# Optimization experiments

Hardware: AMD Instinct MI355X
Metric: run time of the kernel (lower is better)

Reference implementation:

```python
import jax, jax.numpy as jnp
import numpy as np

B, L, D = 2, 2048, 1024
H, DH = 16, 64
HIDDEN = 4096
DILATION, WINDOW, CAUSAL = 2, 512, True
EPS = 1e-5


def _ln(x, g, b):
    m = jnp.mean(x, axis=-1, keepdims=True)
    v = jnp.mean(jnp.square(x - m), axis=-1, keepdims=True)
    return (x - m) * jax.lax.rsqrt(v + EPS) * g + b


def setup_inputs() -> dict:
    key = jax.random.key(0)
    ks = jax.random.split(key, 8)
    s = 0.02
    return {
        "x": jax.random.normal(ks[0], (B, L, D), jnp.float32),
        "ln1_g": jnp.ones((D,), jnp.float32),
        "ln1_b": jnp.zeros((D,), jnp.float32),
        "w_qkv": jax.random.normal(ks[1], (3 * D, D), jnp.float32) * s,
        "b_qkv": jnp.zeros((3 * D,), jnp.float32),
        "w_o": jax.random.normal(ks[2], (D, D), jnp.float32) * s,
        "b_o": jnp.zeros((D,), jnp.float32),
        "ln2_g": jnp.ones((D,), jnp.float32),
        "ln2_b": jnp.zeros((D,), jnp.float32),
        "w_ff1": jax.random.normal(ks[3], (HIDDEN, D), jnp.float32) * s,
        "b_ff1": jnp.zeros((HIDDEN,), jnp.float32),
        "w_ff2": jax.random.normal(ks[4], (D, HIDDEN), jnp.float32) * s,
        "b_ff2": jnp.zeros((D,), jnp.float32),
    }


def reference(x, ln1_g, ln1_b, w_qkv, b_qkv, w_o, b_o, ln2_g, ln2_b, w_ff1, b_ff1, w_ff2, b_ff2):
    # pre-norm attention block with dilated/windowed/causal mask
    h = _ln(x, ln1_g, ln1_b)
    qkv = h @ w_qkv.T + b_qkv                      # [B, L, 3D]
    q, k, v = jnp.split(qkv, 3, axis=-1)
    q = q.reshape(B, L, H, DH)
    k = k.reshape(B, L, H, DH)
    v = v.reshape(B, L, H, DH)

    scale = 1.0 / jnp.sqrt(jnp.float32(DH))
    scores = jnp.einsum("bqhd,bkhd->bhqk", q, k) * scale  # [B, H, L, L]

    i = jnp.arange(L)[:, None]
    j = jnp.arange(L)[None, :]
    allowed = ((i - j) % DILATION == 0) & (jnp.abs(i - j) <= WINDOW)
    if CAUSAL:
        allowed = allowed & (j <= i)
    scores = jnp.where(allowed, scores, -jnp.inf)  # diagonal always allowed -> rows finite

    p = jax.nn.softmax(scores, axis=-1)
    attn = jnp.einsum("bhqk,bkhd->bqhd", p, v).reshape(B, L, D)

    out = x + attn @ w_o.T + b_o                   # residual 1 (dropout p=0)

    h2 = _ln(out, ln2_g, ln2_b)
    ff = jax.nn.gelu(h2 @ w_ff1.T + b_ff1, approximate=False) @ w_ff2.T + b_ff2
    return out + ff                                # residual 2
```

## Files before the change

kernel.cpp:

```cpp
#include <hip/hip_runtime.h>
#include <hip/hip_bf16.h>
#include <cmath>

#define Bsz 2
#define Lseq 2048
#define Dmod 1024
#define Hhead 16
#define DH 64
#define HID 4096
#define ROWS (Bsz * Lseq)
#define TD (3 * Dmod)

typedef __attribute__((ext_vector_type(8))) short bf16x8;
typedef __attribute__((ext_vector_type(4))) float f32x4;
typedef unsigned short ushort_t;

typedef const __attribute__((address_space(1))) void gv_t;
typedef __attribute__((address_space(3))) void lv_t;
#define GLDS16(GP, LP) __builtin_amdgcn_global_load_lds((gv_t*)(GP), (lv_t*)(LP), 16, 0, 0)

__device__ __forceinline__ float bf2f(short u)
{
    return __uint_as_float(((unsigned)(unsigned short)u) << 16);
}
__device__ __forceinline__ unsigned pack2(float a, float b)
{
    __hip_bfloat162 t;
    t.x = __float2bfloat16(a);
    t.y = __float2bfloat16(b);
    return *reinterpret_cast<unsigned*>(&t);
}
__device__ __forceinline__ float gelu_exact(float t)
{
    return 0.5f * t * (1.0f + erff(t * 0.70710678118654752f));
}

__device__ __forceinline__ void xcd_remap(int& mblk, int& nblk)
{
    int nx = gridDim.x;
    int nwg = nx * gridDim.y;
    int id = blockIdx.y * nx + blockIdx.x;
    int cpx = nwg >> 3;
    int swz = (id & 7) * cpx + (id >> 3);
    mblk = swz / nx;
    nblk = swz % nx;
}

__global__ __launch_bounds__(256) void f2b_kernel(const float* __restrict__ in,
                                                  ushort_t* __restrict__ out, int n4)
{
    int i = blockIdx.x * 256 + threadIdx.x;
    if (i >= n4) return;
    float4 v = reinterpret_cast<const float4*>(in)[i];
    uint2 o;
    o.x = pack2(v.x, v.y);
    o.y = pack2(v.z, v.w);
    reinterpret_cast<uint2*>(out)[i] = o;
}

__global__ __launch_bounds__(256) void ln_kernel(const float* __restrict__ x,
                                                 const float* __restrict__ g,
                                                 const float* __restrict__ bta,
                                                 ushort_t* __restrict__ out)
{
    int row = blockIdx.x;
    int t = threadIdx.x;
    const float4* xr = reinterpret_cast<const float4*>(x) + (size_t)row * 256;
    float4 v = xr[t];
    float s  = v.x + v.y + v.z + v.w;
    float s2 = v.x * v.x + v.y * v.y + v.z * v.z + v.w * v.w;
#pragma unroll
    for (int o = 32; o > 0; o >>= 1) {
        s  += __shfl_down(s, o);
        s2 += __shfl_down(s2, o);
    }
    __shared__ float sa[4], sb[4];
    int wv = t >> 6, ln = t & 63;
    if (ln == 0) { sa[wv] = s; sb[wv] = s2; }
    __syncthreads();
    s  = sa[0] + sa[1] + sa[2] + sa[3];
    s2 = sb[0] + sb[1] + sb[2] + sb[3];
    float mean = s * (1.0f / 1024.0f);
    float var  = s2 * (1.0f / 1024.0f) - mean * mean;
    float inv  = rsqrtf(var + 1e-5f);
    float4 gv = reinterpret_cast<const float4*>(g)[t];
    float4 bv = reinterpret_cast<const float4*>(bta)[t];
    uint2 o;
    o.x = pack2((v.x - mean) * inv * gv.x + bv.x, (v.y - mean) * inv * gv.y + bv.y);
    o.y = pack2((v.z - mean) * inv * gv.z + bv.z, (v.w - mean) * inv * gv.w + bv.w);
    reinterpret_cast<uint2*>(out)[(size_t)row * 256 + t] = o;
}

__global__ __launch_bounds__(256) void gemm_bt(const ushort_t* __restrict__ A,
                                               const ushort_t* __restrict__ W,
                                               const float* __restrict__ bias,
                                               const float* __restrict__ res,
                                               void* __restrict__ C,
                                               int M, int N, int K, int ldw,
                                               int act, int obf)
{
    __shared__ ushort_t As[128 * 64];
    __shared__ ushort_t Bs[128 * 64];

    int tid = threadIdx.x;
    int w = tid >> 6, lane = tid & 63;
    int mblk, nblk;
    xcd_remap(mblk, nblk);
    int m0 = mblk * 128, n0 = nblk * 128;
    int wr = (w >> 1) * 64, wc = (w & 1) * 64;

    int srow = lane >> 3;
    int scol = (((lane & 7) ^ (lane >> 3)) & 7) * 8;
    const ushort_t* ga[4];
    const ushort_t* gb[4];
    ushort_t* la[4];
    ushort_t* lb[4];
#pragma unroll
    for (int q = 0; q < 4; ++q) {
        ga[q] = A + (size_t)(m0 + w * 32 + q * 8 + srow) * K + scol;
        gb[q] = W + (size_t)(n0 + w * 32 + q * 8 + srow) * ldw + scol;
        la[q] = As + (w * 32 + q * 8) * 64;
        lb[q] = Bs + (w * 32 + q * 8) * 64;
    }

    int fr = lane & 15;
    int fg = lane >> 4;
    int r0 = fg * 4;
    int cc = fr;

    f32x4 acc[4][4] = {};

    for (int k0 = 0; k0 < K; k0 += 64) {
#pragma unroll
        for (int q = 0; q < 4; ++q) {
            GLDS16(ga[q] + k0, la[q]);
            GLDS16(gb[q] + k0, lb[q]);
        }
        __syncthreads();

#pragma unroll
        for (int kk = 0; kk < 2; ++kk) {
            bf16x8 af[4], bfr[4];
#pragma unroll
            for (int i = 0; i < 4; ++i) {
                int ca = ((kk * 4 + fg) ^ (fr & 7)) * 8;
                af[i]  = *reinterpret_cast<const bf16x8*>(&As[(wr + i * 16 + fr) * 64 + ca]);
                bfr[i] = *reinterpret_cast<const bf16x8*>(&Bs[(wc + i * 16 + fr) * 64 + ca]);
            }
#pragma unroll
            for (int mi = 0; mi < 4; ++mi)
#pragma unroll
                for (int ni = 0; ni < 4; ++ni)
                    acc[mi][ni] = __builtin_amdgcn_mfma_f32_16x16x32_bf16(
                        af[mi], bfr[ni], acc[mi][ni], 0, 0, 0);
        }
        __syncthreads();
    }

    float bv[4];
#pragma unroll
    for (int ni = 0; ni < 4; ++ni)
        bv[ni] = bias ? bias[n0 + wc + ni * 16 + cc] : 0.0f;

#pragma unroll
    for (int mi = 0; mi < 4; ++mi) {
#pragma unroll
        for (int r = 0; r < 4; ++r) {
            int row = m0 + wr + mi * 16 + r0 + r;
            const float* resrow = res ? res + (size_t)row * N : nullptr;
#pragma unroll
            for (int ni = 0; ni < 4; ++ni) {
                int col = n0 + wc + ni * 16 + cc;
                float v = acc[mi][ni][r] + bv[ni];
                if (act == 1) v = gelu_exact(v);
                if (resrow) v += resrow[col];
                if (obf) {
                    reinterpret_cast<ushort_t*>(C)[(size_t)row * N + col] =
                        (ushort_t)__bfloat16_as_ushort(__float2bfloat16(v));
                } else {
                    reinterpret_cast<float*>(C)[(size_t)row * N + col] = v;
                }
            }
        }
    }
}

__global__ __launch_bounds__(256) void gemm_n64(const ushort_t* __restrict__ A,
                                                const ushort_t* __restrict__ W,
                                                const float* __restrict__ bias,
                                                const float* __restrict__ res,
                                                void* __restrict__ C,
                                                int M, int N, int K, int ldw,
                                                int act, int obf)
{
    __shared__ ushort_t As[128 * 64];
    __shared__ ushort_t Bs[64 * 64];

    int tid = threadIdx.x;
    int w = tid >> 6, lane = tid & 63;
    int mblk, nblk;
    xcd_remap(mblk, nblk);
    int m0 = mblk * 128, n0 = nblk * 64;
    int wr = (w >> 1) * 64, wc = (w & 1) * 32;

    int srow = lane >> 3;
    int scol = (((lane & 7) ^ (lane >> 3)) & 7) * 8;
    const ushort_t* ga[4];
    const ushort_t* gb[2];
    ushort_t* la[4];
    ushort_t* lb[2];
#pragma unroll
    for (int q = 0; q < 4; ++q) {
        ga[q] = A + (size_t)(m0 + w * 32 + q * 8 + srow) * K + scol;
        la[q] = As + (w * 32 + q * 8) * 64;
    }
#pragma unroll
    for (int q = 0; q < 2; ++q) {
        gb[q] = W + (size_t)(n0 + w * 16 + q * 8 + srow) * ldw + scol;
        lb[q] = Bs + (w * 16 + q * 8) * 64;
    }

    int fr = lane & 15;
    int fg = lane >> 4;
    int r0 = fg * 4;
    int cc = fr;

    f32x4 acc[4][2] = {};

    for (int k0 = 0; k0 < K; k0 += 64) {
#pragma unroll
        for (int q = 0; q < 4; ++q) GLDS16(ga[q] + k0, la[q]);
#pragma unroll
        for (int q = 0; q < 2; ++q) GLDS16(gb[q] + k0, lb[q]);
        __syncthreads();

#pragma unroll
        for (int kk = 0; kk < 2; ++kk) {
            bf16x8 af[4], bfr[2];
            int ca = ((kk * 4 + fg) ^ (fr & 7)) * 8;
#pragma unroll
            for (int i = 0; i < 4; ++i)
                af[i] = *reinterpret_cast<const bf16x8*>(&As[(wr + i * 16 + fr) * 64 + ca]);
#pragma unroll
            for (int i = 0; i < 2; ++i)
                bfr[i] = *reinterpret_cast<const bf16x8*>(&Bs[(wc + i * 16 + fr) * 64 + ca]);
#pragma unroll
            for (int mi = 0; mi < 4; ++mi)
#pragma unroll
                for (int ni = 0; ni < 2; ++ni)
                    acc[mi][ni] = __builtin_amdgcn_mfma_f32_16x16x32_bf16(
                        af[mi], bfr[ni], acc[mi][ni], 0, 0, 0);
        }
        __syncthreads();
    }

    float bv[2];
#pragma unroll
    for (int ni = 0; ni < 2; ++ni)
        bv[ni] = bias ? bias[n0 + wc + ni * 16 + cc] : 0.0f;

#pragma unroll
    for (int mi = 0; mi < 4; ++mi) {
#pragma unroll
        for (int r = 0; r < 4; ++r) {
            int row = m0 + wr + mi * 16 + r0 + r;
            const float* resrow = res ? res + (size_t)row * N : nullptr;
#pragma unroll
            for (int ni = 0; ni < 2; ++ni) {
                int col = n0 + wc + ni * 16 + cc;
                float v = acc[mi][ni][r] + bv[ni];
                if (act == 1) v = gelu_exact(v);
                if (resrow) v += resrow[col];
                if (obf) {
                    reinterpret_cast<ushort_t*>(C)[(size_t)row * N + col] =
                        (ushort_t)__bfloat16_as_ushort(__float2bfloat16(v));
                } else {
                    reinterpret_cast<float*>(C)[(size_t)row * N + col] = v;
                }
            }
        }
    }
}

__global__ __launch_bounds__(256) void attn_mfma(const ushort_t* __restrict__ qkv,
                                                 ushort_t* __restrict__ out)
{
    __shared__ ushort_t Vt[64][328];
    __shared__ ushort_t Pw[4][16][40];

    int bid = blockIdx.x;
    int qt = bid & 15, h = (bid >> 4) & 15, p = (bid >> 8) & 1, b = bid >> 9;
    int qt0 = qt * 64;
    int kstart = qt0 - 256;

    const ushort_t* base = qkv + (size_t)b * Lseq * TD;
    int tid = threadIdx.x;

#pragma unroll
    for (int it = 0; it < 10; ++it) {
        int idx = it * 256 + tid;
        int ko = idx >> 3;
        int dg = idx & 7;
        int kk = kstart + ko;
        bf16x8 v = {};
        if (kk >= 0)
            v = *reinterpret_cast<const bf16x8*>(base + (size_t)(2 * kk + p) * TD + 2048 + h * 64 + dg * 8);
#pragma unroll
        for (int j = 0; j < 8; ++j)
            Vt[dg * 8 + j][ko] = (ushort_t)v[j];
    }

    int w = tid >> 6, lane = tid & 63;
    int fr = lane & 15, fg = lane >> 4;
    int qw = qt0 + w * 16;
    const ushort_t* qrow = base + (size_t)(2 * (qw + fr) + p) * TD + h * 64;
    bf16x8 qf0 = *reinterpret_cast<const bf16x8*>(qrow + fg * 8);
    bf16x8 qf1 = *reinterpret_cast<const bf16x8*>(qrow + 32 + fg * 8);

    __syncthreads();

    float m[4]    = {-1e30f, -1e30f, -1e30f, -1e30f};
    float lsum[4] = {};
    f32x4 o[4]    = {};
    const float scale = 0.125f;
    int qbase = qw + fg * 4;

    for (int t = 0; t < 10; ++t) {
        int kt0 = kstart + t * 32;
        int kk0 = kt0 + fr, kk1 = kk0 + 16;
        int kk0c = kk0 < 0 ? 0 : kk0;
        int kk1c = kk1 < 0 ? 0 : kk1;
        const ushort_t* kr0 = base + (size_t)(2 * kk0c + p) * TD + 1024 + h * 64;
        const ushort_t* kr1 = base + (size_t)(2 * kk1c + p) * TD + 1024 + h * 64;
        bf16x8 k00 = *reinterpret_cast<const bf16x8*>(kr0 + fg * 8);
        bf16x8 k01 = *reinterpret_cast<const bf16x8*>(kr0 + 32 + fg * 8);
        bf16x8 k10 = *reinterpret_cast<const bf16x8*>(kr1 + fg * 8);
        bf16x8 k11 = *reinterpret_cast<const bf16x8*>(kr1 + 32 + fg * 8);

        f32x4 s0 = {}, s1 = {};
        s0 = __builtin_amdgcn_mfma_f32_16x16x32_bf16(qf0, k00, s0, 0, 0, 0);
        s0 = __builtin_amdgcn_mfma_f32_16x16x32_bf16(qf1, k01, s0, 0, 0, 0);
        s1 = __builtin_amdgcn_mfma_f32_16x16x32_bf16(qf0, k10, s1, 0, 0, 0);
        s1 = __builtin_amdgcn_mfma_f32_16x16x32_bf16(qf1, k11, s1, 0, 0, 0);

        int c0 = kt0 + fr, c1 = c0 + 16;
        float v0[4], v1[4], tmax[4];
#pragma unroll
        for (int r = 0; r < 4; ++r) {
            int qq = qbase + r;
            bool a0 = (c0 >= 0) && (c0 <= qq) && (c0 >= qq - 256);
            bool a1 = (c1 >= 0) && (c1 <= qq) && (c1 >= qq - 256);
            v0[r] = a0 ? s0[r] * scale : -1e30f;
            v1[r] = a1 ? s1[r] * scale : -1e30f;
            tmax[r] = fmaxf(v0[r], v1[r]);
        }
#pragma unroll
        for (int off = 1; off < 16; off <<= 1) {
#pragma unroll
            for (int r = 0; r < 4; ++r)
                tmax[r] = fmaxf(tmax[r], __shfl_xor(tmax[r], off));
        }
#pragma unroll
        for (int r = 0; r < 4; ++r) {
            float mn = fmaxf(m[r], tmax[r]);
            float corr = __expf(m[r] - mn);
            m[r] = mn;
            float p0 = __expf(v0[r] - mn);
            float p1 = __expf(v1[r] - mn);
            lsum[r] = lsum[r] * corr + p0 + p1;
#pragma unroll
            for (int db = 0; db < 4; ++db)
                o[db][r] *= corr;
            Pw[w][fg * 4 + r][fr]      = (ushort_t)__bfloat16_as_ushort(__float2bfloat16(p0));
            Pw[w][fg * 4 + r][fr + 16] = (ushort_t)__bfloat16_as_ushort(__float2bfloat16(p1));
        }

        bf16x8 pf = *reinterpret_cast<const bf16x8*>(&Pw[w][fr][fg * 8]);
#pragma unroll
        for (int db = 0; db < 4; ++db) {
            bf16x8 vf = *reinterpret_cast<const bf16x8*>(&Vt[db * 16 + fr][t * 32 + fg * 8]);
            o[db] = __builtin_amdgcn_mfma_f32_16x16x32_bf16(pf, vf, o[db], 0, 0, 0);
        }
    }

#pragma unroll
    for (int off = 1; off < 16; off <<= 1) {
#pragma unroll
        for (int r = 0; r < 4; ++r)
            lsum[r] += __shfl_xor(lsum[r], off);
    }
    float inv[4];
#pragma unroll
    for (int r = 0; r < 4; ++r) inv[r] = 1.0f / lsum[r];

#pragma unroll
    for (int r = 0; r < 4; ++r) {
        size_t orow = ((size_t)b * Lseq + 2 * (qbase + r) + p) * Dmod + h * 64;
#pragma unroll
        for (int db = 0; db < 4; ++db)
            out[orow + db * 16 + fr] =
                (ushort_t)__bfloat16_as_ushort(__float2bfloat16(o[db][r] * inv[r]));
    }
}

extern "C" void kernel_launch(void* const* d_in, const int* in_sizes, int n_in,
                              void* d_out, int out_size, void* d_ws, size_t ws_size,
                              hipStream_t stream)
{
    const float* x     = (const float*)d_in[0];
    const float* ln1_g = (const float*)d_in[1];
    const float* ln1_b = (const float*)d_in[2];
    const float* w_qkv = (const float*)d_in[3];
    const float* b_qkv = (const float*)d_in[4];
    const float* w_o   = (const float*)d_in[5];
    const float* b_o   = (const float*)d_in[6];
    const float* ln2_g = (const float*)d_in[7];
    const float* ln2_b = (const float*)d_in[8];
    const float* w_ff1 = (const float*)d_in[9];
    const float* b_ff1 = (const float*)d_in[10];
    const float* w_ff2 = (const float*)d_in[11];
    const float* b_ff2 = (const float*)d_in[12];
    float* out = (float*)d_out;

    ushort_t* wq     = (ushort_t*)d_ws;
    ushort_t* wo     = wq  + (size_t)TD * Dmod;
    ushort_t* wf1    = wo  + (size_t)Dmod * Dmod;
    ushort_t* wf2    = wf1 + (size_t)HID * Dmod;
    ushort_t* bufFF  = wf2 + (size_t)Dmod * HID;
    ushort_t* bufH   = bufFF + (size_t)ROWS * HID;
    ushort_t* bufAtt = bufH + (size_t)ROWS * Dmod;

    f2b_kernel<<<(TD * Dmod / 4 + 255) / 256, 256, 0, stream>>>(w_qkv, wq, TD * Dmod / 4);
    f2b_kernel<<<(Dmod * Dmod / 4 + 255) / 256, 256, 0, stream>>>(w_o, wo, Dmod * Dmod / 4);
    f2b_kernel<<<(HID * Dmod / 4 + 255) / 256, 256, 0, stream>>>(w_ff1, wf1, HID * Dmod / 4);
    f2b_kernel<<<(Dmod * HID / 4 + 255) / 256, 256, 0, stream>>>(w_ff2, wf2, Dmod * HID / 4);

    ln_kernel<<<ROWS, 256, 0, stream>>>(x, ln1_g, ln1_b, bufH);
    gemm_bt<<<dim3(TD / 128, ROWS / 128), 256, 0, stream>>>(bufH, wq, b_qkv, nullptr,
                                                            bufFF, ROWS, TD, Dmod, Dmod, 0, 1);
    attn_mfma<<<Bsz * 2 * Hhead * (1024 / 64), 256, 0, stream>>>(bufFF, bufAtt);
    gemm_n64<<<dim3(Dmod / 64, ROWS / 128), 256, 0, stream>>>(bufAtt, wo, b_o, x,
                                                              out, ROWS, Dmod, Dmod, Dmod, 0, 0);
    ln_kernel<<<ROWS, 256, 0, stream>>>(out, ln2_g, ln2_b, bufH);
    gemm_bt<<<dim3(HID / 128, ROWS / 128), 256, 0, stream>>>(bufH, wf1, b_ff1, nullptr,
                                                             bufFF, ROWS, HID, Dmod, Dmod, 1, 1);
    gemm_n64<<<dim3(Dmod / 64, ROWS / 128), 256, 0, stream>>>(bufFF, wf2, b_ff2, out,
                                                              out, ROWS, Dmod, HID, HID, 0, 0);
}
```

Measured before the change: 264.5 us.

## Double-buffer LDS in GEMM kernels and merge weight conversions into one launch

Both GEMM kernels now use two LDS buffers, so the global-to-LDS load of the next K tile is issued before the MFMA compute on the current tile, overlapping memory latency with compute. The four fp32-to-bf16 weight conversion launches are merged into one kernel that picks its source and destination by block index. This doubles LDS use per block, which can lower occupancy, and relies on K being a multiple of 128.

```diff
diff --git a/kernel.cpp b/kernel.cpp
--- a/kernel.cpp
+++ b/kernel.cpp
@@ -46,16 +46,25 @@
     nblk = swz % nx;
 }
 
-__global__ __launch_bounds__(256) void f2b_kernel(const float* __restrict__ in,
-                                                  ushort_t* __restrict__ out, int n4)
-{
-    int i = blockIdx.x * 256 + threadIdx.x;
-    if (i >= n4) return;
-    float4 v = reinterpret_cast<const float4*>(in)[i];
+__global__ __launch_bounds__(256) void f2b4_kernel(const float* __restrict__ s0, ushort_t* __restrict__ d0,
+                                                   const float* __restrict__ s1, ushort_t* __restrict__ d1,
+                                                   const float* __restrict__ s2, ushort_t* __restrict__ d2,
+                                                   const float* __restrict__ s3, ushort_t* __restrict__ d3)
+{
+    int blk = blockIdx.x;
+    const float* src;
+    ushort_t* dst;
+    int base;
+    if (blk < 3072)      { src = s0; dst = d0; base = blk; }
+    else if (blk < 4096) { src = s1; dst = d1; base = blk - 3072; }
+    else if (blk < 8192) { src = s2; dst = d2; base = blk - 4096; }
+    else                 { src = s3; dst = d3; base = blk - 8192; }
+    int i = base * 256 + threadIdx.x;
+    float4 v = reinterpret_cast<const float4*>(src)[i];
     uint2 o;
     o.x = pack2(v.x, v.y);
     o.y = pack2(v.z, v.w);
-    reinterpret_cast<uint2*>(out)[i] = o;
+    reinterpret_cast<uint2*>(dst)[i] = o;
 }
 
 __global__ __launch_bounds__(256) void ln_kernel(const float* __restrict__ x,
@@ -99,8 +108,10 @@
                                                int M, int N, int K, int ldw,
                                                int act, int obf)
 {
-    __shared__ ushort_t As[128 * 64];
-    __shared__ ushort_t Bs[128 * 64];
+    __shared__ ushort_t As0[128 * 64];
+    __shared__ ushort_t Bs0[128 * 64];
+    __shared__ ushort_t As1[128 * 64];
+    __shared__ ushort_t Bs1[128 * 64];
 
     int tid = threadIdx.x;
     int w = tid >> 6, lane = tid & 63;
@@ -113,14 +124,12 @@
     int scol = (((lane & 7) ^ (lane >> 3)) & 7) * 8;
     const ushort_t* ga[4];
     const ushort_t* gb[4];
-    ushort_t* la[4];
-    ushort_t* lb[4];
+    int lofs[4];
 #pragma unroll
     for (int q = 0; q < 4; ++q) {
         ga[q] = A + (size_t)(m0 + w * 32 + q * 8 + srow) * K + scol;
         gb[q] = W + (size_t)(n0 + w * 32 + q * 8 + srow) * ldw + scol;
-        la[q] = As + (w * 32 + q * 8) * 64;
-        lb[q] = Bs + (w * 32 + q * 8) * 64;
+        lofs[q] = (w * 32 + q * 8) * 64;
     }
 
     int fr = lane & 15;
@@ -130,22 +139,22 @@
 
     f32x4 acc[4][4] = {};
 
-    for (int k0 = 0; k0 < K; k0 += 64) {
+    auto stage = [&](ushort_t* AS, ushort_t* BS, int k0) {
 #pragma unroll
         for (int q = 0; q < 4; ++q) {
-            GLDS16(ga[q] + k0, la[q]);
-            GLDS16(gb[q] + k0, lb[q]);
-        }
-        __syncthreads();
-
+            GLDS16(ga[q] + k0, AS + lofs[q]);
+            GLDS16(gb[q] + k0, BS + lofs[q]);
+        }
+    };
+    auto compute = [&](const ushort_t* AS, const ushort_t* BS) {
 #pragma unroll
         for (int kk = 0; kk < 2; ++kk) {
             bf16x8 af[4], bfr[4];
+            int ca = ((kk * 4 + fg) ^ (fr & 7)) * 8;
 #pragma unroll
             for (int i = 0; i < 4; ++i) {
-                int ca = ((kk * 4 + fg) ^ (fr & 7)) * 8;
-                af[i]  = *reinterpret_cast<const bf16x8*>(&As[(wr + i * 16 + fr) * 64 + ca]);
-                bfr[i] = *reinterpret_cast<const bf16x8*>(&Bs[(wc + i * 16 + fr) * 64 + ca]);
+                af[i]  = *reinterpret_cast<const bf16x8*>(&AS[(wr + i * 16 + fr) * 64 + ca]);
+                bfr[i] = *reinterpret_cast<const bf16x8*>(&BS[(wc + i * 16 + fr) * 64 + ca]);
             }
 #pragma unroll
             for (int mi = 0; mi < 4; ++mi)
@@ -154,6 +163,17 @@
                     acc[mi][ni] = __builtin_amdgcn_mfma_f32_16x16x32_bf16(
                         af[mi], bfr[ni], acc[mi][ni], 0, 0, 0);
         }
+    };
+
+    int nt = K >> 6;
+    stage(As0, Bs0, 0);
+    __syncthreads();
+    for (int t = 0; t < nt; t += 2) {
+        stage(As1, Bs1, (t + 1) * 64);
+        compute(As0, Bs0);
+        __syncthreads();
+        if (t + 2 < nt) stage(As0, Bs0, (t + 2) * 64);
+        compute(As1, Bs1);
         __syncthreads();
     }
 
@@ -193,8 +213,10 @@
                                                 int M, int N, int K, int ldw,
                                                 int act, int obf)
 {
-    __shared__ ushort_t As[128 * 64];
-    __shared__ ushort_t Bs[64 * 64];
+    __shared__ ushort_t As0[128 * 64];
+    __shared__ ushort_t Bs0[64 * 64];
+    __shared__ ushort_t As1[128 * 64];
+    __shared__ ushort_t Bs1[64 * 64];
 
     int tid = threadIdx.x;
     int w = tid >> 6, lane = tid & 63;
@@ -207,17 +229,16 @@
     int scol = (((lane & 7) ^ (lane >> 3)) & 7) * 8;
     const ushort_t* ga[4];
     const ushort_t* gb[2];
-    ushort_t* la[4];
-    ushort_t* lb[2];
+    int laofs[4], lbofs[2];
 #pragma unroll
     for (int q = 0; q < 4; ++q) {
         ga[q] = A + (size_t)(m0 + w * 32 + q * 8 + srow) * K + scol;
-        la[q] = As + (w * 32 + q * 8) * 64;
+        laofs[q] = (w * 32 + q * 8) * 64;
     }
 #pragma unroll
     for (int q = 0; q < 2; ++q) {
         gb[q] = W + (size_t)(n0 + w * 16 + q * 8 + srow) * ldw + scol;
-        lb[q] = Bs + (w * 16 + q * 8) * 64;
+        lbofs[q] = (w * 16 + q * 8) * 64;
     }
 
     int fr = lane & 15;
@@ -227,23 +248,23 @@
 
     f32x4 acc[4][2] = {};
 
-    for (int k0 = 0; k0 < K; k0 += 64) {
-#pragma unroll
-        for (int q = 0; q < 4; ++q) GLDS16(ga[q] + k0, la[q]);
-#pragma unroll
-        for (int q = 0; q < 2; ++q) GLDS16(gb[q] + k0, lb[q]);
-        __syncthreads();
-
+    auto stage = [&](ushort_t* AS, ushort_t* BS, int k0) {
+#pragma unroll
+        for (int q = 0; q < 4; ++q) GLDS16(ga[q] + k0, AS + laofs[q]);
+#pragma unroll
+        for (int q = 0; q < 2; ++q) GLDS16(gb[q] + k0, BS + lbofs[q]);
+    };
+    auto compute = [&](const ushort_t* AS, const ushort_t* BS) {
 #pragma unroll
         for (int kk = 0; kk < 2; ++kk) {
             bf16x8 af[4], bfr[2];
             int ca = ((kk * 4 + fg) ^ (fr & 7)) * 8;
 #pragma unroll
             for (int i = 0; i < 4; ++i)
-                af[i] = *reinterpret_cast<const bf16x8*>(&As[(wr + i * 16 + fr) * 64 + ca]);
+                af[i] = *reinterpret_cast<const bf16x8*>(&AS[(wr + i * 16 + fr) * 64 + ca]);
 #pragma unroll
             for (int i = 0; i < 2; ++i)
-                bfr[i] = *reinterpret_cast<const bf16x8*>(&Bs[(wc + i * 16 + fr) * 64 + ca]);
+                bfr[i] = *reinterpret_cast<const bf16x8*>(&BS[(wc + i * 16 + fr) * 64 + ca]);
 #pragma unroll
             for (int mi = 0; mi < 4; ++mi)
 #pragma unroll
@@ -251,6 +272,17 @@
                     acc[mi][ni] = __builtin_amdgcn_mfma_f32_16x16x32_bf16(
                         af[mi], bfr[ni], acc[mi][ni], 0, 0, 0);
         }
+    };
+
+    int nt = K >> 6;
+    stage(As0, Bs0, 0);
+    __syncthreads();
+    for (int t = 0; t < nt; t += 2) {
+        stage(As1, Bs1, (t + 1) * 64);
+        compute(As0, Bs0);
+        __syncthreads();
+        if (t + 2 < nt) stage(As0, Bs0, (t + 2) * 64);
+        compute(As1, Bs1);
         __syncthreads();
     }
 
@@ -430,10 +462,7 @@
     ushort_t* bufH   = bufFF + (size_t)ROWS * HID;
     ushort_t* bufAtt = bufH + (size_t)ROWS * Dmod;
 
-    f2b_kernel<<<(TD * Dmod / 4 + 255) / 256, 256, 0, stream>>>(w_qkv, wq, TD * Dmod / 4);
-    f2b_kernel<<<(Dmod * Dmod / 4 + 255) / 256, 256, 0, stream>>>(w_o, wo, Dmod * Dmod / 4);
-    f2b_kernel<<<(HID * Dmod / 4 + 255) / 256, 256, 0, stream>>>(w_ff1, wf1, HID * Dmod / 4);
-    f2b_kernel<<<(Dmod * HID / 4 + 255) / 256, 256, 0, stream>>>(w_ff2, wf2, Dmod * HID / 4);
+    f2b4_kernel<<<12288, 256, 0, stream>>>(w_qkv, wq, w_o, wo, w_ff1, wf1, w_ff2, wf2);
 
     ln_kernel<<<ROWS, 256, 0, stream>>>(x, ln1_g, ln1_b, bufH);
     gemm_bt<<<dim3(TD / 128, ROWS / 128), 256, 0, stream>>>(bufH, wq, b_qkv, nullptr,
```

Measured after the change: 246.2 us. -6.9%, faster.
